# Optimization experiments

Hardware: AMD Instinct MI355X
Metric: run time of the kernel (lower is better)

## Reference

```python
import jax, jax.numpy as jnp
import numpy as np

D, H, B = 512, 8, 64
NF, NO = 16384, 8192
EPS = 1e-5


def _ln(x):
    m = jnp.mean(x, axis=-1, keepdims=True)
    v = jnp.mean((x - m) ** 2, axis=-1, keepdims=True)
    return (x - m) / jnp.sqrt(v + EPS)


def setup_inputs() -> dict:
    key = jax.random.key(0)
    ks = jax.random.split(key, 16)
    s = 1.0 / np.sqrt(D)
    inp = {
        "hf": jax.random.normal(ks[0], (NF, D), jnp.float32),
        "ho": jax.random.normal(ks[1], (NO, D), jnp.float32),
        "ps": jax.random.normal(ks[2], (B, D), jnp.float32),
        "face_batch": jnp.sort(jax.random.randint(ks[3], (NF,), 0, B)),
        "obj_batch": jnp.sort(jax.random.randint(ks[4], (NO,), 0, B)),
        "Wq": jax.random.normal(ks[5], (D, D), jnp.float32) * s,
        "bq": jnp.zeros((D,), jnp.float32),
        "Wk": jax.random.normal(ks[6], (D, D), jnp.float32) * s,
        "bk": jnp.zeros((D,), jnp.float32),
        "Wv": jax.random.normal(ks[7], (D, D), jnp.float32) * s,
        "bv": jnp.zeros((D,), jnp.float32),
        "Wo": jax.random.normal(ks[8], (D, D), jnp.float32) * s,
        "bo": jnp.zeros((D,), jnp.float32),
        "Wg": jax.random.normal(ks[9], (D, D), jnp.float32) * s,
        "bg": jnp.full((D,), -1.0, jnp.float32),  # init.constant_(bias, -1.0)
        "alpha": jax.random.normal(ks[10], (D,), jnp.float32) * 0.1,
    }
    return inp


def reference(hf, ho, ps, face_batch, obj_batch, Wq, bq, Wk, bk, Wv, bv, Wo, bo, Wg, bg, alpha):
    dh = D // H
    nodes = jnp.concatenate([hf, ho], axis=0)            # (N, D)
    seg = jnp.concatenate([face_batch, obj_batch], 0)    # (N,)
    N = nodes.shape[0]

    # single-query cross-attention done as ragged/segment attention
    # (identical math to padded MHA with key_padding_mask)
    q = (ps @ Wq + bq).reshape(B, H, dh)                 # (B, H, dh)
    k = (nodes @ Wk + bk).reshape(N, H, dh)
    v = (nodes @ Wv + bv).reshape(N, H, dh)

    scores = jnp.einsum("nhd,nhd->nh", k, q[seg]) / np.sqrt(dh)   # (N, H)
    mx = jax.ops.segment_max(scores, seg, num_segments=B)          # (B, H)
    e = jnp.exp(scores - mx[seg])                                  # (N, H)
    denom = jax.ops.segment_sum(e, seg, num_segments=B)            # (B, H)
    num = jax.ops.segment_sum(e[:, :, None] * v, seg, num_segments=B)  # (B, H, dh)
    attn = (num / denom[:, :, None]).reshape(B, D)
    attn_out = attn @ Wo + bo

    fs = _ln(ps + attn_out)                               # (B, D)
    gate = jax.nn.sigmoid(hf @ Wg + bg)                   # (NF, D)
    signal = alpha * fs[face_batch]                       # (NF, D)
    hf_new = _ln(hf + gate * signal)
    return hf_new, fs
```

## Files before the change

### kernel.cpp

```cpp
#include <hip/hip_runtime.h>
#include <hip/hip_bf16.h>
#include <math.h>

constexpr int D  = 512;
constexpr int H  = 8;
constexpr int DH = 64;
constexpr int B  = 64;
constexpr int NF = 16384;
constexpr int NO = 8192;
constexpr int NT = NF + NO;
constexpr float EPS = 1e-5f;
constexpr float LOG2E = 1.4426950408889634f;

constexpr int PREP_PK   = 512;
constexpr int PREP_BND  = PREP_PK;
constexpr int PREP_WG0  = PREP_BND + 1;
constexpr int PREP_CVT0 = PREP_WG0 + 256;
constexpr int CVT_BLOCKS = NT * D / 2048;
constexpr int PREP_TOTAL = PREP_CVT0 + CVT_BLOCKS;

typedef short short8 __attribute__((ext_vector_type(8)));
typedef float f32x4 __attribute__((ext_vector_type(4)));
typedef unsigned short ushort;
typedef ushort ushort8v __attribute__((ext_vector_type(8)));

__device__ __forceinline__ ushort f2bf(float f) {
  unsigned int x = __float_as_uint(f);
  x += 0x7FFF + ((x >> 16) & 1);
  return (ushort)(x >> 16);
}
__device__ __forceinline__ float bf2f(ushort u) {
  return __uint_as_float(((unsigned int)u) << 16);
}
__device__ __forceinline__ float fast_exp(float x) {
  return __builtin_amdgcn_exp2f(x * LOG2E);
}
__device__ __forceinline__ float fast_sigmoid(float z) {
  return __builtin_amdgcn_rcpf(1.0f + __builtin_amdgcn_exp2f(-z * LOG2E));
}
__device__ __forceinline__ short8 cvt8(float4 f0, float4 f1) {
  union { short8 v; __hip_bfloat162 h[4]; } u;
  u.h[0] = __float22bfloat162_rn(float2{f0.x, f0.y});
  u.h[1] = __float22bfloat162_rn(float2{f0.z, f0.w});
  u.h[2] = __float22bfloat162_rn(float2{f1.x, f1.y});
  u.h[3] = __float22bfloat162_rn(float2{f1.z, f1.w});
  return u.v;
}
__device__ __forceinline__ void gll16(const void* g, void* l) {
  __builtin_amdgcn_global_load_lds(
      (const __attribute__((address_space(1))) void*)g,
      (__attribute__((address_space(3))) void*)l, 16, 0, 0);
}

__global__ __launch_bounds__(256) void k_prep(const float* __restrict__ ps,
                                              const float* __restrict__ Wq,
                                              const float* __restrict__ bq,
                                              const float* __restrict__ Wk,
                                              const float* __restrict__ bk,
                                              const float* __restrict__ Wg,
                                              const float* __restrict__ hf,
                                              const float* __restrict__ ho,
                                              const int* __restrict__ fb,
                                              const int* __restrict__ ob,
                                              float* __restrict__ Pk,
                                              float* __restrict__ qbk,
                                              ushort* __restrict__ Wgt,
                                              ushort* __restrict__ nodesb,
                                              int* __restrict__ fstart,
                                              int* __restrict__ ostart) {
  __shared__ float shm[1056];
  const int bid = blockIdx.x, t = threadIdx.x;
  if (bid < PREP_PK) {
    const int b = bid >> 3, h = bid & 7;
    for (int i = t; i < D; i += 256) shm[i] = ps[(size_t)b * D + i];
    __syncthreads();
    {
      const int j = t >> 2, eq = t & 3;
      const int col = h * 64 + j;
      float acc = 0.f;
      const float* wp = Wq + (size_t)(eq * 128) * D + col;
      #pragma unroll 8
      for (int e = 0; e < 128; ++e) acc += shm[eq * 128 + e] * wp[(size_t)e * D];
      acc += __shfl_xor(acc, 1); acc += __shfl_xor(acc, 2);
      if (eq == 0) shm[512 + j] = acc + bq[col];
    }
    __syncthreads();
    for (int e = t; e < D; e += 256) {
      float acc = 0.f;
      #pragma unroll 8
      for (int j = 0; j < DH; ++j) acc += Wk[(size_t)e * D + h * DH + j] * shm[512 + j];
      Pk[((size_t)b * H + h) * D + e] = acc;
    }
    if (t == 0) {
      float s = 0.f;
      for (int j = 0; j < DH; ++j) s += bk[h * DH + j] * shm[512 + j];
      qbk[b * H + h] = s;
    }
  } else if (bid == PREP_BND) {
    if (t <= B) {
      int lo = 0, hi = NF;
      while (lo < hi) { int mid = (lo + hi) >> 1; if (fb[mid] < t) lo = mid + 1; else hi = mid; }
      fstart[t] = lo;
    } else if (t >= 128 && t <= 128 + B) {
      int v = t - 128;
      int lo = 0, hi = NO;
      while (lo < hi) { int mid = (lo + hi) >> 1; if (ob[mid] < v) lo = mid + 1; else hi = mid; }
      ostart[v] = lo;
    }
  } else if (bid < PREP_CVT0) {
    float (*tile)[33] = (float(*)[33])shm;
    const int tb = bid - PREP_WG0;
    const int bx = tb & 15, by = tb >> 4;
    const int tx = t & 31, ty = t >> 5;
    #pragma unroll
    for (int i = 0; i < 4; ++i)
      tile[ty + i * 8][tx] = Wg[(size_t)(by * 32 + ty + i * 8) * D + bx * 32 + tx];
    __syncthreads();
    #pragma unroll
    for (int i = 0; i < 4; ++i)
      Wgt[(size_t)(bx * 32 + ty + i * 8) * D + by * 32 + tx] = f2bf(tile[tx][ty + i * 8]);
  } else {
    size_t idx = (size_t)(bid - PREP_CVT0) * 2048 + (size_t)t * 8;
    const float* src = (idx < (size_t)NF * D) ? (hf + idx) : (ho + (idx - (size_t)NF * D));
    float4 f0 = *(const float4*)src, f1 = *(const float4*)(src + 4);
    *(short8*)(nodesb + idx) = cvt8(f0, f1);
  }
}

__global__ __launch_bounds__(256) void k_gate(const ushort* __restrict__ hfb,
                                              const ushort* __restrict__ Wgt,
                                              const float* __restrict__ bg,
                                              ushort* __restrict__ gateb) {
  __shared__ ushort Asb[2][4096];
  __shared__ ushort Bs[2][4096];
  const int tid = threadIdx.x, lane = tid & 63, w = tid >> 6;
  const int rowBase = blockIdx.x * 128, colBase = blockIdx.y * 128;
  const int wm = w >> 1, wn = w & 1;
  const int lrow = lane & 15, kg = lane >> 4;

  int ra[2], ca[2], cb[2], cc[2];
  #pragma unroll
  for (int j = 0; j < 2; ++j) {
    int ia = (w * 2 + j) * 64 + lane;
    ra[j] = ia >> 2;
    ca[j] = (ia & 3) ^ ((ra[j] >> 1) & 3);
    cb[j] = ra[j];
    cc[j] = ca[j];
  }

#define STAGE(buf, k0)                                                          \
  {                                                                             \
    _Pragma("unroll")                                                           \
    for (int j = 0; j < 2; ++j)                                                 \
      gll16(hfb + (size_t)(rowBase + ra[j]) * D + (k0) + ca[j] * 8,             \
            &Asb[buf][(w * 2 + j) * 512]);                                      \
    _Pragma("unroll")                                                           \
    for (int j = 0; j < 2; ++j)                                                 \
      gll16(Wgt + (size_t)(colBase + cb[j]) * D + (k0) + cc[j] * 8,             \
            &Bs[buf][(w * 2 + j) * 512]);                                       \
  }

  STAGE(0, 0);
  __syncthreads();

  f32x4 acc[4][4] = {};
  for (int t = 0; t < 16; ++t) {
    const int cur = t & 1;
    if (t < 15) STAGE(cur ^ 1, (t + 1) * 32);
    short8 av[4], bv[4];
    #pragma unroll
    for (int m = 0; m < 4; ++m) {
      const int a_r = wm * 64 + m * 16 + lrow;
      av[m] = *(const short8*)&Asb[cur][a_r * 32 + (kg ^ ((a_r >> 1) & 3)) * 8];
    }
    #pragma unroll
    for (int n = 0; n < 4; ++n) {
      const int b_c = wn * 64 + n * 16 + lrow;
      bv[n] = *(const short8*)&Bs[cur][b_c * 32 + (kg ^ ((b_c >> 1) & 3)) * 8];
    }
    #pragma unroll
    for (int m = 0; m < 4; ++m)
      #pragma unroll
      for (int n = 0; n < 4; ++n)
        acc[m][n] = __builtin_amdgcn_mfma_f32_16x16x32_bf16(av[m], bv[n], acc[m][n], 0, 0, 0);
    __syncthreads();
  }
#undef STAGE

  #pragma unroll
  for (int n = 0; n < 4; ++n) {
    const int col = colBase + wn * 64 + n * 16 + lrow;
    const float bgv = bg[col];
    #pragma unroll
    for (int m = 0; m < 4; ++m) {
      const int row0 = rowBase + wm * 64 + m * 16 + kg * 4;
      #pragma unroll
      for (int r = 0; r < 4; ++r)
        gateb[(size_t)(row0 + r) * D + col] = f2bf(fast_sigmoid(acc[m][n][r] + bgv));
    }
  }
}

__global__ __launch_bounds__(256) void k_scores(const ushort* __restrict__ nodesb,
                                                const int* __restrict__ fb,
                                                const int* __restrict__ ob,
                                                const float* __restrict__ Pk,
                                                const float* __restrict__ qbk,
                                                float* __restrict__ scores) {
  int lane = threadIdx.x & 63;
  int n = blockIdx.x * 4 + (threadIdx.x >> 6);
  int b = (n < NF) ? fb[n] : ob[n - NF];
  union { short8 v; ushort u[8]; } ux;
  ux.v = *(const short8*)(nodesb + (size_t)n * D + lane * 8);
  float xf[8];
  #pragma unroll
  for (int i = 0; i < 8; ++i) xf[i] = bf2f(ux.u[i]);
  float acc[H];
  #pragma unroll
  for (int h = 0; h < H; ++h) {
    const float4* p4 = (const float4*)(Pk + ((size_t)b * H + h) * D) + lane * 2;
    float4 p0 = p4[0], p1 = p4[1];
    acc[h] = xf[0] * p0.x + xf[1] * p0.y + xf[2] * p0.z + xf[3] * p0.w +
             xf[4] * p1.x + xf[5] * p1.y + xf[6] * p1.z + xf[7] * p1.w;
  }
  #pragma unroll
  for (int h = 0; h < H; ++h) {
    float v = acc[h];
    #pragma unroll
    for (int off = 32; off; off >>= 1) v += __shfl_xor(v, off);
    if (lane == h) scores[(size_t)n * H + h] = (v + qbk[b * H + h]) * 0.125f;
  }
}

__global__ __launch_bounds__(512) void k_segsoftmax(const float* __restrict__ scores,
                                                    const int* __restrict__ fstart,
                                                    const int* __restrict__ ostart,
                                                    float* __restrict__ evals,
                                                    float* __restrict__ denom) {
  int b = blockIdx.x;
  int h = threadIdx.x >> 6, lane = threadIdx.x & 63;
  int f0 = fstart[b], f1 = fstart[b + 1];
  int o0 = ostart[b], o1 = ostart[b + 1];
  float m = -1e30f;
  for (int i = f0 + lane; i < f1; i += 64) m = fmaxf(m, scores[(size_t)i * H + h]);
  for (int i = o0 + lane; i < o1; i += 64) m = fmaxf(m, scores[(size_t)(NF + i) * H + h]);
  #pragma unroll
  for (int off = 32; off; off >>= 1) m = fmaxf(m, __shfl_xor(m, off));
  float s = 0.f;
  for (int i = f0 + lane; i < f1; i += 64) {
    float e = fast_exp(scores[(size_t)i * H + h] - m);
    evals[(size_t)i * H + h] = e; s += e;
  }
  for (int i = o0 + lane; i < o1; i += 64) {
    float e = fast_exp(scores[(size_t)(NF + i) * H + h] - m);
    evals[(size_t)(NF + i) * H + h] = e; s += e;
  }
  #pragma unroll
  for (int off = 32; off; off >>= 1) s += __shfl_xor(s, off);
  if (lane == 0) denom[b * H + h] = s;
}

__global__ __launch_bounds__(512) void k_Taccum(const ushort* __restrict__ nodesb,
                                                const int* __restrict__ fstart,
                                                const int* __restrict__ ostart,
                                                const float* __restrict__ evals,
                                                float* __restrict__ T8) {
  int b = blockIdx.x, chunk = blockIdx.y;
  int e = threadIdx.x;
  int f0 = fstart[b], flen = fstart[b + 1] - f0;
  int o0 = ostart[b], olen = ostart[b + 1] - o0;
  int L = flen + olen;
  float acc[8] = {0.f, 0.f, 0.f, 0.f, 0.f, 0.f, 0.f, 0.f};
  for (int idx = chunk; idx < L; idx += 8) {
    int n = (idx < flen) ? (f0 + idx) : (NF + o0 + (idx - flen));
    float x = bf2f(nodesb[(size_t)n * D + e]);
    const float4* ev = (const float4*)(evals + (size_t)n * H);
    float4 e0 = ev[0], e1 = ev[1];
    acc[0] += e0.x * x; acc[1] += e0.y * x; acc[2] += e0.z * x; acc[3] += e0.w * x;
    acc[4] += e1.x * x; acc[5] += e1.y * x; acc[6] += e1.z * x; acc[7] += e1.w * x;
  }
  #pragma unroll
  for (int h = 0; h < H; ++h)
    T8[(((size_t)chunk * B + b) * H + h) * D + e] = acc[h];
}

__global__ __launch_bounds__(256) void k_attn(const float* __restrict__ T8,
                                              const float* __restrict__ denom,
                                              const float* __restrict__ Wv,
                                              const float* __restrict__ bv,
                                              float* __restrict__ attn) {
  __shared__ float Ts[D];
  int b = blockIdx.x, h = blockIdx.y, t = threadIdx.x;
  for (int i = t; i < D; i += 256) {
    float s = 0.f;
    #pragma unroll
    for (int c2 = 0; c2 < 8; ++c2)
      s += T8[(((size_t)c2 * B + b) * H + h) * D + i];
    Ts[i] = s;
  }
  __syncthreads();
  int col = h * DH + (t >> 2), eq = t & 3;
  float acc = 0.f;
  const float* wp = Wv + (size_t)(eq * 128) * D + col;
  #pragma unroll 8
  for (int e = 0; e < 128; ++e) acc += Ts[eq * 128 + e] * wp[(size_t)e * D];
  acc += __shfl_xor(acc, 1); acc += __shfl_xor(acc, 2);
  if (eq == 0) attn[(size_t)b * D + col] = acc / denom[b * H + h] + bv[col];
}

__global__ __launch_bounds__(256) void k_x(const float* __restrict__ attn,
                                           const float* __restrict__ Wo,
                                           const float* __restrict__ bo,
                                           const float* __restrict__ ps,
                                           float* __restrict__ x) {
  __shared__ float As[D];
  int b = blockIdx.x, cg = blockIdx.y, t = threadIdx.x;
  for (int i = t; i < D; i += 256) As[i] = attn[(size_t)b * D + i];
  __syncthreads();
  int col = cg * 64 + (t >> 2), eq = t & 3;
  float acc = 0.f;
  const float* wp = Wo + (size_t)(eq * 128) * D + col;
  #pragma unroll 8
  for (int e = 0; e < 128; ++e) acc += As[eq * 128 + e] * wp[(size_t)e * D];
  acc += __shfl_xor(acc, 1); acc += __shfl_xor(acc, 2);
  if (eq == 0) x[(size_t)b * D + col] = acc + bo[col] + ps[(size_t)b * D + col];
}

__global__ __launch_bounds__(512) void k_ln(const float* __restrict__ x,
                                            float* __restrict__ fs) {
  __shared__ float redS[8], redQ[8];
  __shared__ float sM, sI;
  int b = blockIdx.x, t = threadIdx.x;
  float v = x[(size_t)b * D + t];
  float s = v, sq = v * v;
  #pragma unroll
  for (int off = 32; off; off >>= 1) { s += __shfl_xor(s, off); sq += __shfl_xor(sq, off); }
  int wv = t >> 6, ln = t & 63;
  if (ln == 0) { redS[wv] = s; redQ[wv] = sq; }
  __syncthreads();
  if (t == 0) {
    float S = 0.f, Q = 0.f;
    #pragma unroll
    for (int i = 0; i < 8; ++i) { S += redS[i]; Q += redQ[i]; }
    float mean = S * (1.f / D);
    float var = Q * (1.f / D) - mean * mean;
    sM = mean; sI = rsqrtf(var + EPS);
  }
  __syncthreads();
  fs[(size_t)b * D + t] = (v - sM) * sI;
}

__global__ __launch_bounds__(256) void k_final(const ushort* __restrict__ hfb,
                                               const ushort* __restrict__ gateb,
                                               const float* __restrict__ alpha,
                                               const float* __restrict__ fs,
                                               const int* __restrict__ fb,
                                               float* __restrict__ out) {
  const int w = threadIdx.x >> 6, lane = threadIdx.x & 63;
  const int row = blockIdx.x * 4 + w;
  const int b = fb[row];
  const ushort* hr = hfb + (size_t)row * D + lane * 8;
  const ushort* gr = gateb + (size_t)row * D + lane * 8;
  const float* fr = fs + (size_t)b * D + lane * 8;
  const float* ar = alpha + lane * 8;
  union { ushort8v v; ushort u[8]; } uh, ug;
  uh.v = *(const ushort8v*)hr;
  ug.v = *(const ushort8v*)gr;
  float4 p0 = *(const float4*)fr, p1 = *(const float4*)(fr + 4);
  float4 a0 = *(const float4*)ar, a1 = *(const float4*)(ar + 4);
  float pv[8] = {p0.x, p0.y, p0.z, p0.w, p1.x, p1.y, p1.z, p1.w};
  float av[8] = {a0.x, a0.y, a0.z, a0.w, a1.x, a1.y, a1.z, a1.w};
  float x[8], s = 0.f, sq = 0.f;
  #pragma unroll
  for (int i = 0; i < 8; ++i) {
    x[i] = bf2f(uh.u[i]) + bf2f(ug.u[i]) * (av[i] * pv[i]);
    s += x[i]; sq += x[i] * x[i];
  }
  #pragma unroll
  for (int off = 32; off; off >>= 1) { s += __shfl_xor(s, off); sq += __shfl_xor(sq, off); }
  float mean = s * (1.f / D);
  float inv = rsqrtf(sq * (1.f / D) - mean * mean + EPS);
  float* op = out + (size_t)row * D + lane * 8;
  float4 o0 = {(x[0] - mean) * inv, (x[1] - mean) * inv, (x[2] - mean) * inv, (x[3] - mean) * inv};
  float4 o1 = {(x[4] - mean) * inv, (x[5] - mean) * inv, (x[6] - mean) * inv, (x[7] - mean) * inv};
  *(float4*)op = o0;
  *(float4*)(op + 4) = o1;
}

extern "C" void kernel_launch(void* const* d_in, const int* in_sizes, int n_in,
                              void* d_out, int out_size, void* d_ws, size_t ws_size,
                              hipStream_t stream) {
  const float* hf    = (const float*)d_in[0];
  const float* ho    = (const float*)d_in[1];
  const float* ps    = (const float*)d_in[2];
  const int*   fb    = (const int*)d_in[3];
  const int*   ob    = (const int*)d_in[4];
  const float* Wq    = (const float*)d_in[5];
  const float* bq    = (const float*)d_in[6];
  const float* Wk    = (const float*)d_in[7];
  const float* bk    = (const float*)d_in[8];
  const float* Wv    = (const float*)d_in[9];
  const float* bv    = (const float*)d_in[10];
  const float* Wo    = (const float*)d_in[11];
  const float* bo    = (const float*)d_in[12];
  const float* Wg    = (const float*)d_in[13];
  const float* bg    = (const float*)d_in[14];
  const float* alpha = (const float*)d_in[15];

  float* out    = (float*)d_out;
  float* fs_out = out + (size_t)NF * D;

  ushort* Wgt    = (ushort*)d_ws;
  ushort* gateb  = Wgt + 512 * 512;
  ushort* nodesb = gateb + (size_t)NF * D;
  float* fbase   = (float*)(nodesb + (size_t)NT * D);
  float* Pk     = fbase;
  float* qbk    = Pk + B * H * D;
  float* scores = qbk + B * H;
  float* evals  = scores + (size_t)NT * H;
  float* denom  = evals + (size_t)NT * H;
  float* T8     = denom + B * H;
  float* attn   = T8 + (size_t)8 * B * H * D;
  float* xbuf   = attn + B * D;
  int* fstart   = (int*)(xbuf + B * D);
  int* ostart   = fstart + (B + 1);

  k_prep<<<PREP_TOTAL, 256, 0, stream>>>(ps, Wq, bq, Wk, bk, Wg, hf, ho, fb, ob,
                                         Pk, qbk, Wgt, nodesb, fstart, ostart);
  k_gate<<<dim3(NF / 128, 4), 256, 0, stream>>>(nodesb, Wgt, bg, gateb);
  k_scores<<<NT / 4, 256, 0, stream>>>(nodesb, fb, ob, Pk, qbk, scores);
  k_segsoftmax<<<B, 512, 0, stream>>>(scores, fstart, ostart, evals, denom);
  k_Taccum<<<dim3(B, 8), 512, 0, stream>>>(nodesb, fstart, ostart, evals, T8);
  k_attn<<<dim3(B, H), 256, 0, stream>>>(T8, denom, Wv, bv, attn);
  k_x<<<dim3(B, 8), 256, 0, stream>>>(attn, Wo, bo, ps, xbuf);
  k_ln<<<B, 512, 0, stream>>>(xbuf, fs_out);
  k_final<<<NF / 4, 256, 0, stream>>>(nodesb, gateb, alpha, fs_out, fb, out);
}
```

Measured before the change: 130.3 us.

## Fuse attention tail stages into one cooperative persistent kernel with grid syncs

Replaces seven separate launches (scores, segment softmax, T accumulation, attention projection, output projection, layernorm, final gated layernorm) with a single cooperative kernel. It uses grid-stride loops and grid.sync between stages, sized from occupancy and capped at 1024 blocks. The aim is to remove per-launch overhead and the gaps between small kernels. In exchange, several stages now run with fewer blocks or with changed work splits (softmax at 256 threads instead of 512, T accumulation split in halves), and each grid barrier has a cost. The old launch sequence is kept as a fallback if the cooperative launch fails.

```diff
diff --git a/kernel.cpp b/kernel.cpp
--- a/kernel.cpp
+++ b/kernel.cpp
@@ -1,6 +1,9 @@
 #include <hip/hip_runtime.h>
 #include <hip/hip_bf16.h>
+#include <hip/hip_cooperative_groups.h>
 #include <math.h>
+
+namespace cgrp = cooperative_groups;
 
 constexpr int D  = 512;
 constexpr int H  = 8;
@@ -387,6 +390,192 @@
   *(float4*)(op + 4) = o1;
 }
 
+__global__ __launch_bounds__(256, 4) void k_coop(
+    const ushort* __restrict__ nodesb,
+    const int* __restrict__ fb, const int* __restrict__ ob,
+    const float* __restrict__ Pk, const float* __restrict__ qbk,
+    float* __restrict__ scores,
+    const int* __restrict__ fstart, const int* __restrict__ ostart,
+    float* __restrict__ evals, float* __restrict__ denom,
+    float* __restrict__ T8,
+    const float* __restrict__ Wv, const float* __restrict__ bv,
+    float* __restrict__ attn,
+    const float* __restrict__ Wo, const float* __restrict__ bo,
+    const float* __restrict__ ps,
+    float* __restrict__ xbuf,
+    float* __restrict__ fs,
+    const ushort* __restrict__ gateb,
+    const float* __restrict__ alpha,
+    float* __restrict__ out) {
+  cgrp::grid_group grid = cgrp::this_grid();
+  const int G = gridDim.x;
+  const int bid = blockIdx.x, t = threadIdx.x;
+  const int lane = t & 63, w = t >> 6;
+  __shared__ float shm[544];
+
+  for (int g = bid; g < NT / 4; g += G) {
+    int n = g * 4 + w;
+    int b = (n < NF) ? fb[n] : ob[n - NF];
+    union { short8 v; ushort u[8]; } ux;
+    ux.v = *(const short8*)(nodesb + (size_t)n * D + lane * 8);
+    float xf[8];
+    #pragma unroll
+    for (int i = 0; i < 8; ++i) xf[i] = bf2f(ux.u[i]);
+    float acc[H];
+    #pragma unroll
+    for (int h = 0; h < H; ++h) {
+      const float4* p4 = (const float4*)(Pk + ((size_t)b * H + h) * D) + lane * 2;
+      float4 p0 = p4[0], p1 = p4[1];
+      acc[h] = xf[0] * p0.x + xf[1] * p0.y + xf[2] * p0.z + xf[3] * p0.w +
+               xf[4] * p1.x + xf[5] * p1.y + xf[6] * p1.z + xf[7] * p1.w;
+    }
+    #pragma unroll
+    for (int h = 0; h < H; ++h) {
+      float v = acc[h];
+      #pragma unroll
+      for (int off = 32; off; off >>= 1) v += __shfl_xor(v, off);
+      if (lane == h) scores[(size_t)n * H + h] = (v + qbk[b * H + h]) * 0.125f;
+    }
+  }
+  grid.sync();
+
+  for (int u = bid; u < B * H; u += G) {
+    __syncthreads();
+    int b = u >> 3, h = u & 7;
+    int f0 = fstart[b], f1 = fstart[b + 1];
+    int o0 = ostart[b], o1 = ostart[b + 1];
+    float m = -1e30f;
+    for (int i = f0 + t; i < f1; i += 256) m = fmaxf(m, scores[(size_t)i * H + h]);
+    for (int i = o0 + t; i < o1; i += 256) m = fmaxf(m, scores[(size_t)(NF + i) * H + h]);
+    #pragma unroll
+    for (int off = 32; off; off >>= 1) m = fmaxf(m, __shfl_xor(m, off));
+    if (lane == 0) shm[512 + w] = m;
+    __syncthreads();
+    m = fmaxf(fmaxf(shm[512], shm[513]), fmaxf(shm[514], shm[515]));
+    float s = 0.f;
+    for (int i = f0 + t; i < f1; i += 256) {
+      float e = fast_exp(scores[(size_t)i * H + h] - m);
+      evals[(size_t)i * H + h] = e; s += e;
+    }
+    for (int i = o0 + t; i < o1; i += 256) {
+      float e = fast_exp(scores[(size_t)(NF + i) * H + h] - m);
+      evals[(size_t)(NF + i) * H + h] = e; s += e;
+    }
+    #pragma unroll
+    for (int off = 32; off; off >>= 1) s += __shfl_xor(s, off);
+    if (lane == 0) shm[520 + w] = s;
+    __syncthreads();
+    if (t == 0) denom[b * H + h] = shm[520] + shm[521] + shm[522] + shm[523];
+  }
+  grid.sync();
+
+  for (int u = bid; u < B * 16; u += G) {
+    int b = u >> 4, chunk = (u >> 1) & 7, half = u & 1;
+    int e = half * 256 + t;
+    int f0 = fstart[b], flen = fstart[b + 1] - f0;
+    int o0 = ostart[b], olen = ostart[b + 1] - o0;
+    int L = flen + olen;
+    float acc[8] = {0.f, 0.f, 0.f, 0.f, 0.f, 0.f, 0.f, 0.f};
+    for (int idx = chunk; idx < L; idx += 8) {
+      int n = (idx < flen) ? (f0 + idx) : (NF + o0 + (idx - flen));
+      float x = bf2f(nodesb[(size_t)n * D + e]);
+      const float4* ev = (const float4*)(evals + (size_t)n * H);
+      float4 e0 = ev[0], e1 = ev[1];
+      acc[0] += e0.x * x; acc[1] += e0.y * x; acc[2] += e0.z * x; acc[3] += e0.w * x;
+      acc[4] += e1.x * x; acc[5] += e1.y * x; acc[6] += e1.z * x; acc[7] += e1.w * x;
+    }
+    #pragma unroll
+    for (int h = 0; h < H; ++h)
+      T8[(((size_t)chunk * B + b) * H + h) * D + e] = acc[h];
+  }
+  grid.sync();
+
+  for (int u = bid; u < B * H; u += G) {
+    __syncthreads();
+    int b = u >> 3, h = u & 7;
+    for (int i = t; i < D; i += 256) {
+      float s = 0.f;
+      #pragma unroll
+      for (int c2 = 0; c2 < 8; ++c2)
+        s += T8[(((size_t)c2 * B + b) * H + h) * D + i];
+      shm[i] = s;
+    }
+    __syncthreads();
+    int col = h * DH + (t >> 2), eq = t & 3;
+    float acc = 0.f;
+    const float* wp = Wv + (size_t)(eq * 128) * D + col;
+    #pragma unroll 8
+    for (int e = 0; e < 128; ++e) acc += shm[eq * 128 + e] * wp[(size_t)e * D];
+    acc += __shfl_xor(acc, 1); acc += __shfl_xor(acc, 2);
+    if (eq == 0) attn[(size_t)b * D + col] = acc / denom[b * H + h] + bv[col];
+  }
+  grid.sync();
+
+  for (int u = bid; u < B * 8; u += G) {
+    __syncthreads();
+    int b = u >> 3, cg = u & 7;
+    for (int i = t; i < D; i += 256) shm[i] = attn[(size_t)b * D + i];
+    __syncthreads();
+    int col = cg * 64 + (t >> 2), eq = t & 3;
+    float acc = 0.f;
+    const float* wp = Wo + (size_t)(eq * 128) * D + col;
+    #pragma unroll 8
+    for (int e = 0; e < 128; ++e) acc += shm[eq * 128 + e] * wp[(size_t)e * D];
+    acc += __shfl_xor(acc, 1); acc += __shfl_xor(acc, 2);
+    if (eq == 0) xbuf[(size_t)b * D + col] = acc + bo[col] + ps[(size_t)b * D + col];
+  }
+  grid.sync();
+
+  for (int u = bid; u < B; u += G) {
+    __syncthreads();
+    float v0 = xbuf[(size_t)u * D + t];
+    float v1 = xbuf[(size_t)u * D + t + 256];
+    float s = v0 + v1, sq = v0 * v0 + v1 * v1;
+    #pragma unroll
+    for (int off = 32; off; off >>= 1) { s += __shfl_xor(s, off); sq += __shfl_xor(sq, off); }
+    if (lane == 0) { shm[512 + w] = s; shm[520 + w] = sq; }
+    __syncthreads();
+    float S = shm[512] + shm[513] + shm[514] + shm[515];
+    float Q = shm[520] + shm[521] + shm[522] + shm[523];
+    float mean = S * (1.f / D);
+    float inv = rsqrtf(Q * (1.f / D) - mean * mean + EPS);
+    fs[(size_t)u * D + t] = (v0 - mean) * inv;
+    fs[(size_t)u * D + t + 256] = (v1 - mean) * inv;
+  }
+  grid.sync();
+
+  for (int g = bid; g < NF / 4; g += G) {
+    const int row = g * 4 + w;
+    const int b = fb[row];
+    const ushort* hr = nodesb + (size_t)row * D + lane * 8;
+    const ushort* gr = gateb + (size_t)row * D + lane * 8;
+    const float* fr = fs + (size_t)b * D + lane * 8;
+    const float* ar = alpha + lane * 8;
+    union { ushort8v v; ushort u[8]; } uh, ug;
+    uh.v = *(const ushort8v*)hr;
+    ug.v = *(const ushort8v*)gr;
+    float4 p0 = *(const float4*)fr, p1 = *(const float4*)(fr + 4);
+    float4 a0 = *(const float4*)ar, a1 = *(const float4*)(ar + 4);
+    float pv[8] = {p0.x, p0.y, p0.z, p0.w, p1.x, p1.y, p1.z, p1.w};
+    float av[8] = {a0.x, a0.y, a0.z, a0.w, a1.x, a1.y, a1.z, a1.w};
+    float x[8], s = 0.f, sq = 0.f;
+    #pragma unroll
+    for (int i = 0; i < 8; ++i) {
+      x[i] = bf2f(uh.u[i]) + bf2f(ug.u[i]) * (av[i] * pv[i]);
+      s += x[i]; sq += x[i] * x[i];
+    }
+    #pragma unroll
+    for (int off = 32; off; off >>= 1) { s += __shfl_xor(s, off); sq += __shfl_xor(sq, off); }
+    float mean = s * (1.f / D);
+    float inv = rsqrtf(sq * (1.f / D) - mean * mean + EPS);
+    float* op = out + (size_t)row * D + lane * 8;
+    float4 o0 = {(x[0] - mean) * inv, (x[1] - mean) * inv, (x[2] - mean) * inv, (x[3] - mean) * inv};
+    float4 o1 = {(x[4] - mean) * inv, (x[5] - mean) * inv, (x[6] - mean) * inv, (x[7] - mean) * inv};
+    *(float4*)op = o0;
+    *(float4*)(op + 4) = o1;
+  }
+}
+
 extern "C" void kernel_launch(void* const* d_in, const int* in_sizes, int n_in,
                               void* d_out, int out_size, void* d_ws, size_t ws_size,
                               hipStream_t stream) {
@@ -428,11 +617,35 @@
   k_prep<<<PREP_TOTAL, 256, 0, stream>>>(ps, Wq, bq, Wk, bk, Wg, hf, ho, fb, ob,
                                          Pk, qbk, Wgt, nodesb, fstart, ostart);
   k_gate<<<dim3(NF / 128, 4), 256, 0, stream>>>(nodesb, Wgt, bg, gateb);
-  k_scores<<<NT / 4, 256, 0, stream>>>(nodesb, fb, ob, Pk, qbk, scores);
-  k_segsoftmax<<<B, 512, 0, stream>>>(scores, fstart, ostart, evals, denom);
-  k_Taccum<<<dim3(B, 8), 512, 0, stream>>>(nodesb, fstart, ostart, evals, T8);
-  k_attn<<<dim3(B, H), 256, 0, stream>>>(T8, denom, Wv, bv, attn);
-  k_x<<<dim3(B, 8), 256, 0, stream>>>(attn, Wo, bo, ps, xbuf);
-  k_ln<<<B, 512, 0, stream>>>(xbuf, fs_out);
-  k_final<<<NF / 4, 256, 0, stream>>>(nodesb, gateb, alpha, fs_out, fb, out);
-}
+
+  hipError_t ce = hipErrorUnknown;
+  int dev = 0;
+  if (hipGetDevice(&dev) == hipSuccess) {
+    hipDeviceProp_t prop;
+    int maxAct = 0;
+    if (hipGetDeviceProperties(&prop, dev) == hipSuccess &&
+        hipOccupancyMaxActiveBlocksPerMultiprocessor(
+            &maxAct, reinterpret_cast<const void*>(k_coop), 256, 0) == hipSuccess &&
+        maxAct > 0) {
+      long long cb = (long long)maxAct * prop.multiProcessorCount;
+      if (cb > 1024) cb = 1024;
+      void* cargs[] = {
+        (void*)&nodesb, (void*)&fb, (void*)&ob, (void*)&Pk, (void*)&qbk,
+        (void*)&scores, (void*)&fstart, (void*)&ostart, (void*)&evals, (void*)&denom,
+        (void*)&T8, (void*)&Wv, (void*)&bv, (void*)&attn, (void*)&Wo, (void*)&bo,
+        (void*)&ps, (void*)&xbuf, (void*)&fs_out, (void*)&gateb, (void*)&alpha, (void*)&out
+      };
+      ce = hipLaunchCooperativeKernel(reinterpret_cast<const void*>(k_coop),
+                                      dim3((int)cb), dim3(256), cargs, 0, stream);
+    }
+  }
+  if (ce != hipSuccess) {
+    k_scores<<<NT / 4, 256, 0, stream>>>(nodesb, fb, ob, Pk, qbk, scores);
+    k_segsoftmax<<<B, 512, 0, stream>>>(scores, fstart, ostart, evals, denom);
+    k_Taccum<<<dim3(B, 8), 512, 0, stream>>>(nodesb, fstart, ostart, evals, T8);
+    k_attn<<<dim3(B, H), 256, 0, stream>>>(T8, denom, Wv, bv, attn);
+    k_x<<<dim3(B, 8), 256, 0, stream>>>(attn, Wo, bo, ps, xbuf);
+    k_ln<<<B, 512, 0, stream>>>(xbuf, fs_out);
+    k_final<<<NF / 4, 256, 0, stream>>>(nodesb, gateb, alpha, fs_out, fb, out);
+  }
+}
```

New measurement: 485.5 us. 3.73x slower.
